# Kernel tuning notes

Hardware: AMD Instinct MI355X
Metric: run time of the kernel (lower is better)

The kernel has to match this reference:

```python
import jax, jax.numpy as jnp
import numpy as np

B, S, D, H = 2, 2048, 2048, 16
HD = D // H  # 128


def setup_inputs() -> dict:
    key = jax.random.key(0)
    ks = jax.random.split(key, 5)
    x = jax.random.normal(ks[0], (B, S, D), dtype=jnp.float32)
    scale = 1.0 / np.sqrt(D)
    wq = jax.random.normal(ks[1], (D, D), dtype=jnp.float32) * scale
    wk = jax.random.normal(ks[2], (D, D), dtype=jnp.float32) * scale
    wv = jax.random.normal(ks[3], (D, D), dtype=jnp.float32) * scale
    wo = jax.random.normal(ks[4], (D, D), dtype=jnp.float32) * scale
    # RoPE frequencies: theta = 10000, freqs_cis[t, j] = exp(i * t / theta^(2j/HD))
    inv_freq = 1.0 / (10000.0 ** (jnp.arange(0, HD, 2, dtype=jnp.float32) / HD))  # [HD/2]
    t = jnp.arange(S, dtype=jnp.float32)
    ang = jnp.outer(t, inv_freq)  # [S, HD/2]
    freqs_cos = jnp.cos(ang)
    freqs_sin = jnp.sin(ang)
    # Additive causal mask [S, S]
    neg = jnp.float32(-1e9)
    mask = jnp.triu(jnp.full((S, S), neg, dtype=jnp.float32), k=1)
    return {"x": x, "wq": wq, "wk": wk, "wv": wv, "wo": wo,
            "freqs_cos": freqs_cos, "freqs_sin": freqs_sin,
            "mask": mask, "start_pos": 0}


def _rope(t, cos, sin):
    # t: [B, S, H, HD]; cos/sin: [S, HD/2] broadcast as [1, S, 1, HD/2]
    tr = t.reshape(t.shape[:-1] + (HD // 2, 2))
    xr, xi = tr[..., 0], tr[..., 1]
    c = cos[None, :, None, :]
    s = sin[None, :, None, :]
    out_r = xr * c - xi * s
    out_i = xr * s + xi * c
    return jnp.stack([out_r, out_i], axis=-1).reshape(t.shape)


def reference(x, wq, wk, wv, wo, freqs_cos, freqs_sin, mask, start_pos):
    bsz, seqlen, _ = x.shape
    # nn.Linear: y = x @ W.T
    xq = jnp.einsum('bsd,ed->bse', x, wq).reshape(bsz, seqlen, H, HD)
    xk = jnp.einsum('bsd,ed->bse', x, wk).reshape(bsz, seqlen, H, HD)
    xv = jnp.einsum('bsd,ed->bse', x, wv).reshape(bsz, seqlen, H, HD)
    xq = _rope(xq, freqs_cos, freqs_sin)
    xk = _rope(xk, freqs_cos, freqs_sin)
    # [B, H, S, HD]
    xq = xq.transpose(0, 2, 1, 3)
    xk = xk.transpose(0, 2, 1, 3)
    xv = xv.transpose(0, 2, 1, 3)
    scores = jnp.einsum('bhqd,bhkd->bhqk', xq, xk) / jnp.sqrt(jnp.float32(HD))
    scores = scores + mask[None, None, :, :]
    probs = jax.nn.softmax(scores.astype(jnp.float32), axis=-1).astype(xq.dtype)
    out = jnp.einsum('bhqk,bhkd->bhqd', probs, xv)
    out = out.transpose(0, 2, 1, 3).reshape(bsz, seqlen, H * HD)
    return jnp.einsum('bse,de->bsd', out, wo)
```

## Files before the change

### kernel.cpp

```cpp
#include <hip/hip_runtime.h>


#define SQ 2048
#define DQ 2048
#define HQ 16
#define HDQ 128

typedef short bf16x8 __attribute__((ext_vector_type(8)));
typedef short bf16x4 __attribute__((ext_vector_type(4)));
typedef float f32x4 __attribute__((ext_vector_type(4)));

#define WAITVM4 asm volatile("s_waitcnt vmcnt(4)" ::: "memory")
#define WAITVM0 asm volatile("s_waitcnt vmcnt(0)" ::: "memory")

__device__ __forceinline__ short f2bf(float f) {
  union { float f; unsigned u; } v; v.f = f;
  unsigned r = (v.u + 0x7FFFu + ((v.u >> 16) & 1u)) >> 16;
  return (short)r;
}
__device__ __forceinline__ float bf2f(short b) {
  union { unsigned u; float f; } v; v.u = ((unsigned)(unsigned short)b) << 16;
  return v.f;
}
__device__ __forceinline__ void gload_lds16(const void* g, void* l) {
  __builtin_amdgcn_global_load_lds(
      (const __attribute__((address_space(1))) void*)g,
      (__attribute__((address_space(3))) void*)l, 16, 0, 0);
}

__global__ void cvt_kernel(const float* __restrict__ in, short* __restrict__ out, int nvec) {
  int i = blockIdx.x * blockDim.x + threadIdx.x;
  if (i >= nvec) return;
  const f32x4* p = (const f32x4*)in + (size_t)i * 2;
  f32x4 a = p[0], b = p[1];
  bf16x8 o;
  o[0] = f2bf(a[0]); o[1] = f2bf(a[1]); o[2] = f2bf(a[2]); o[3] = f2bf(a[3]);
  o[4] = f2bf(b[0]); o[5] = f2bf(b[1]); o[6] = f2bf(b[2]); o[7] = f2bf(b[3]);
  *((bf16x8*)out + i) = o;
}

__global__ void rope_kernel(short* __restrict__ t, const float* __restrict__ cosT,
                            const float* __restrict__ sinT, float scale, int nvec) {
  int i = blockIdx.x * blockDim.x + threadIdx.x;
  if (i >= nvec) return;
  size_t off = (size_t)i * 8;
  int hd0 = (int)(off & 127);
  int s = (int)((off >> 7) & 2047);
  bf16x8 v = *((const bf16x8*)(t + off));
  f32x4 c  = *(const f32x4*)(cosT + (size_t)s * 64 + (hd0 >> 1));
  f32x4 sn = *(const f32x4*)(sinT + (size_t)s * 64 + (hd0 >> 1));
  bf16x8 o;
#pragma unroll
  for (int p = 0; p < 4; ++p) {
    float xr = bf2f(v[2 * p]), xi = bf2f(v[2 * p + 1]);
    o[2 * p]     = f2bf((xr * c[p] - xi * sn[p]) * scale);
    o[2 * p + 1] = f2bf((xr * sn[p] + xi * c[p]) * scale);
  }
  *((bf16x8*)(t + off)) = o;
}

__global__ void vtrans_kernel(const short* __restrict__ vb, short* __restrict__ vtb) {
  __shared__ __align__(16) short tile[64][72];
  int bh = blockIdx.z, s0 = blockIdx.y * 64, d0 = blockIdx.x * 64;
  int tid = threadIdx.x;
#pragma unroll
  for (int it = 0; it < 2; ++it) {
    int vi = it * 256 + tid;
    int r = vi >> 3, c8 = (vi & 7) * 8;
    bf16x8 v = *(const bf16x8*)&vb[((size_t)bh * SQ + s0 + r) * HDQ + d0 + c8];
    *(bf16x8*)&tile[r][c8] = v;
  }
  __syncthreads();
#pragma unroll
  for (int it = 0; it < 2; ++it) {
    int vi = it * 256 + tid;
    int d = vi >> 3, s8 = (vi & 7) * 8;
    bf16x8 o;
#pragma unroll
    for (int j = 0; j < 8; ++j) o[j] = tile[s8 + j][d];
    *(bf16x8*)&vtb[((size_t)bh * HDQ + d0 + d) * SQ + s0 + s8] = o;
  }
}

template <int MODE>
__global__ __launch_bounds__(256, 2) void gemm_bt(const short* __restrict__ A,
                                                  const short* __restrict__ W,
                                                  short* __restrict__ oQ, short* __restrict__ oK,
                                                  short* __restrict__ oV, float* __restrict__ oF) {
  const int K = DQ;
  __shared__ __align__(16) short As[128 * 32];
  __shared__ __align__(16) short Bs[128 * 32];
  int n0 = blockIdx.x * 128, m0 = blockIdx.y * 128;
  const short* Bw = (MODE == 0) ? (W + (size_t)blockIdx.z * DQ * DQ) : W;
  int tid = threadIdx.x, w = tid >> 6, lane = tid & 63;
  int wr = w >> 1, wc = w & 1;
  int ar = lane >> 2, acol = (lane & 3) * 8;
  f32x4 acc[4][4] = {};
  int lra = wr * 64 + (lane & 15), lrb = wc * 64 + (lane & 15), kc = (lane >> 4) * 8;
  for (int k0 = 0; k0 < K; k0 += 32) {
    __syncthreads();
#pragma unroll
    for (int i = 0; i < 2; ++i) {
      int c = w * 2 + i;
      int r = c * 16 + ar;
      gload_lds16(A + (size_t)(m0 + r) * K + k0 + acol, &As[c * 512]);
      gload_lds16(Bw + (size_t)(n0 + r) * K + k0 + acol, &Bs[c * 512]);
    }
    __syncthreads();
    bf16x8 af[4], bfr[4];
#pragma unroll
    for (int f = 0; f < 4; ++f) {
      af[f] = *(const bf16x8*)&As[(lra + f * 16) * 32 + kc];
      bfr[f] = *(const bf16x8*)&Bs[(lrb + f * 16) * 32 + kc];
    }
#pragma unroll
    for (int mf = 0; mf < 4; ++mf)
#pragma unroll
      for (int nf = 0; nf < 4; ++nf)
        acc[mf][nf] = __builtin_amdgcn_mfma_f32_16x16x32_bf16(af[mf], bfr[nf], acc[mf][nf], 0, 0, 0);
  }
  short* oT = nullptr;
  if (MODE == 0) oT = (blockIdx.z == 0) ? oQ : (blockIdx.z == 1) ? oK : oV;
#pragma unroll
  for (int mf = 0; mf < 4; ++mf) {
    int mb = m0 + wr * 64 + mf * 16 + (lane >> 4) * 4;
#pragma unroll
    for (int nf = 0; nf < 4; ++nf) {
      int n = n0 + wc * 64 + nf * 16 + (lane & 15);
#pragma unroll
      for (int j = 0; j < 4; ++j) {
        int m = mb + j;
        float v = acc[mf][nf][j];
        if (MODE == 0) {
          int b = m >> 11, s = m & 2047, h = n >> 7, hd = n & 127;
          oT[(((size_t)(b * HQ + h)) * SQ + s) * HDQ + hd] = f2bf(v);
        } else {
          oF[(size_t)m * DQ + n] = v;
        }
      }
    }
  }
}

__device__ __forceinline__ void stage_kv32(const short* kbase, const short* vbase, int k0,
                                           short* KsB, short* VtB, int w, int lane) {
#pragma unroll
  for (int i = 0; i < 2; ++i) {
    int c = i * 4 + w;
    int ch = c * 64 + lane;
    int r = ch >> 4, c8 = (ch & 15) * 8;
    gload_lds16(kbase + (size_t)(k0 + r) * HDQ + (c8 ^ ((r & 7) << 3)), KsB + c * 512);
    int d = ch >> 2, k8 = (ch & 3) * 8;
    gload_lds16(vbase + (size_t)d * SQ + k0 + (k8 ^ (((d >> 1) & 3) << 3)), VtB + c * 512);
  }
}

__global__ __launch_bounds__(256, 4) void flash_kernel(const short* __restrict__ qb,
                                                       const short* __restrict__ kb,
                                                       const short* __restrict__ vtb,
                                                       short* __restrict__ ab) {
  __shared__ __align__(16) short Ks[2][32 * 128];
  __shared__ __align__(16) short Vt[2][128 * 32];
  __shared__ __align__(16) short Pl[4][16 * 32];
  int x = blockIdx.x, bh = blockIdx.y;
  int qt = (bh & 8) ? (31 - x) : x;
  int q0 = qt * 64;
  int tid = threadIdx.x, w = tid >> 6, lane = tid & 63;
  int g = lane >> 4, qcol = lane & 15;
  int qw0 = q0 + w * 16;
  const short* qbase = qb + (size_t)bh * SQ * HDQ;
  const short* kbase = kb + (size_t)bh * SQ * HDQ;
  const short* vbase = vtb + (size_t)bh * HDQ * SQ;
  int b = bh >> 4, h = bh & 15;

  bf16x8 qf[4];
#pragma unroll
  for (int cc = 0; cc < 4; ++cc)
    qf[cc] = *(const bf16x8*)&qbase[(size_t)(qw0 + qcol) * HDQ + cc * 32 + g * 8];

  f32x4 oacc[8] = {};
  float m_st = -1e30f, l_st = 0.f;
  int nt = 2 * qt + 2;
  stage_kv32(kbase, vbase, 0, Ks[0], Vt[0], w, lane);
#pragma unroll 1
  for (int t = 0; t < nt; ++t) {
    int cur = t & 1;
    int k0 = t * 32;
    __builtin_amdgcn_s_barrier();
    if (t + 1 < nt) {
      stage_kv32(kbase, vbase, (t + 1) * 32, Ks[cur ^ 1], Vt[cur ^ 1], w, lane);
      WAITVM4;
    } else {
      WAITVM0;
    }
    __builtin_amdgcn_s_barrier();
    if (k0 > qw0 + 15) continue;
    f32x4 sacc[2] = {};
    __builtin_amdgcn_s_setprio(1);
#pragma unroll
    for (int nf = 0; nf < 2; ++nf) {
      int rk = nf * 16 + qcol;
#pragma unroll
      for (int cc = 0; cc < 4; ++cc) {
        int ck = cc * 32 + g * 8;
        bf16x8 kf = *(const bf16x8*)&Ks[cur][rk * 128 + (ck ^ ((rk & 7) << 3))];
        sacc[nf] = __builtin_amdgcn_mfma_f32_16x16x32_bf16(kf, qf[cc], sacc[nf], 0, 0, 0);
      }
    }
    __builtin_amdgcn_s_setprio(0);
    int q = qw0 + qcol;
    if (k0 + 31 > qw0) {
#pragma unroll
      for (int nf = 0; nf < 2; ++nf)
#pragma unroll
        for (int j = 0; j < 4; ++j) {
          int k = k0 + nf * 16 + g * 4 + j;
          if (k > q) sacc[nf][j] = -1e9f;
        }
    }
    float mt = fmaxf(fmaxf(fmaxf(sacc[0][0], sacc[0][1]), fmaxf(sacc[0][2], sacc[0][3])),
                     fmaxf(fmaxf(sacc[1][0], sacc[1][1]), fmaxf(sacc[1][2], sacc[1][3])));
    mt = fmaxf(mt, __shfl_xor(mt, 16));
    mt = fmaxf(mt, __shfl_xor(mt, 32));
    float mn = fmaxf(m_st, mt);
    float al = exp2f(m_st - mn);
    float p0[4], p1[4];
    float ls = 0.f;
#pragma unroll
    for (int j = 0; j < 4; ++j) { p0[j] = exp2f(sacc[0][j] - mn); ls += p0[j]; }
#pragma unroll
    for (int j = 0; j < 4; ++j) { p1[j] = exp2f(sacc[1][j] - mn); ls += p1[j]; }
    l_st = l_st * al + ls;
    m_st = mn;
    int sw = (qcol & 3) * 8;
    {
      bf16x4 pk;
      pk[0] = f2bf(p0[0]); pk[1] = f2bf(p0[1]); pk[2] = f2bf(p0[2]); pk[3] = f2bf(p0[3]);
      *(bf16x4*)&Pl[w][qcol * 32 + ((g * 4) ^ sw)] = pk;
      pk[0] = f2bf(p1[0]); pk[1] = f2bf(p1[1]); pk[2] = f2bf(p1[2]); pk[3] = f2bf(p1[3]);
      *(bf16x4*)&Pl[w][qcol * 32 + ((16 + g * 4) ^ sw)] = pk;
    }
    f32x4 alv;
    alv[0] = __shfl(al, g * 4 + 0);
    alv[1] = __shfl(al, g * 4 + 1);
    alv[2] = __shfl(al, g * 4 + 2);
    alv[3] = __shfl(al, g * 4 + 3);
#pragma unroll
    for (int df = 0; df < 8; ++df) oacc[df] *= alv;
    bf16x8 pf = *(const bf16x8*)&Pl[w][qcol * 32 + ((g * 8) ^ sw)];
    __builtin_amdgcn_s_setprio(1);
#pragma unroll
    for (int df = 0; df < 8; ++df) {
      int rd = df * 16 + qcol;
      bf16x8 vf = *(const bf16x8*)&Vt[cur][rd * 32 + ((g * 8) ^ (((rd >> 1) & 3) << 3))];
      oacc[df] = __builtin_amdgcn_mfma_f32_16x16x32_bf16(pf, vf, oacc[df], 0, 0, 0);
    }
    __builtin_amdgcn_s_setprio(0);
  }
  l_st += __shfl_xor(l_st, 16);
  l_st += __shfl_xor(l_st, 32);
  float inv = 1.0f / l_st;
  f32x4 invv;
  invv[0] = __shfl(inv, g * 4 + 0);
  invv[1] = __shfl(inv, g * 4 + 1);
  invv[2] = __shfl(inv, g * 4 + 2);
  invv[3] = __shfl(inv, g * 4 + 3);
#pragma unroll
  for (int df = 0; df < 8; ++df)
#pragma unroll
    for (int j = 0; j < 4; ++j) {
      int qq = qw0 + g * 4 + j;
      int dd = df * 16 + qcol;
      ab[((size_t)b * SQ + qq) * DQ + h * HDQ + dd] = f2bf(oacc[df][j] * invv[j]);
    }
}

extern "C" void kernel_launch(void* const* d_in, const int* in_sizes, int n_in,
                              void* d_out, int out_size, void* d_ws, size_t ws_size,
                              hipStream_t stream) {
  (void)in_sizes; (void)n_in; (void)out_size; (void)ws_size;
  const float* x  = (const float*)d_in[0];
  const float* wq = (const float*)d_in[1];
  const float* wk = (const float*)d_in[2];
  const float* wv = (const float*)d_in[3];
  const float* wo = (const float*)d_in[4];
  const float* fc = (const float*)d_in[5];
  const float* fs = (const float*)d_in[6];
  float* out = (float*)d_out;

  short* xb  = (short*)d_ws;
  short* wqb = xb + (size_t)8388608;
  short* wkb = wqb + (size_t)4194304;
  short* wvb = wkb + (size_t)4194304;
  short* wob = wvb + (size_t)4194304;
  short* qb  = wob + (size_t)4194304;
  short* kb  = qb + (size_t)8388608;
  short* ab  = kb + (size_t)8388608;
  short* vb  = (short*)d_out;
  short* vtb = vb + (size_t)8388608;

  cvt_kernel<<<4096, 256, 0, stream>>>(x, xb, 1048576);
  cvt_kernel<<<2048, 256, 0, stream>>>(wq, wqb, 524288);
  cvt_kernel<<<2048, 256, 0, stream>>>(wk, wkb, 524288);
  cvt_kernel<<<2048, 256, 0, stream>>>(wv, wvb, 524288);
  cvt_kernel<<<2048, 256, 0, stream>>>(wo, wob, 524288);

  gemm_bt<0><<<dim3(16, 32, 3), 256, 0, stream>>>(xb, wqb, qb, kb, vb, nullptr);

  rope_kernel<<<4096, 256, 0, stream>>>(qb, fc, fs, 0.12751744779976827f, 1048576);
  rope_kernel<<<4096, 256, 0, stream>>>(kb, fc, fs, 1.0f, 1048576);

  vtrans_kernel<<<dim3(2, 32, 32), 256, 0, stream>>>(vb, vtb);

  flash_kernel<<<dim3(32, 32), 256, 0, stream>>>(qb, kb, vtb, ab);

  gemm_bt<1><<<dim3(16, 32, 1), 256, 0, stream>>>(ab, wob, nullptr, nullptr, nullptr, out);
}
```

Baseline: 308.8 us.

## Restructure projection GEMMs into 8-wave double-buffered 128x256 tiles with swizzled LDS

Replaces the 4-wave 128x128 GEMM, which used BK=32 and two barriers per step, with a 512-thread kernel computing 128x256 tiles at BK=64. Shared memory is double-buffered so the next K tile loads while the current one computes, synchronised with vmcnt waits. An XOR swizzle on the LDS layout avoids bank conflicts, and s_setprio is raised around the MFMA bursts. This targets global-load latency and LDS stalls in the QKV and output projections. The cost is one block per CU, fewer blocks overall, and more LDS per block.

```diff
diff --git a/kernel.cpp b/kernel.cpp
--- a/kernel.cpp
+++ b/kernel.cpp
@@ -10,6 +10,7 @@
 typedef short bf16x4 __attribute__((ext_vector_type(4)));
 typedef float f32x4 __attribute__((ext_vector_type(4)));
 
+#define WAITVM6 asm volatile("s_waitcnt vmcnt(6)" ::: "memory")
 #define WAITVM4 asm volatile("s_waitcnt vmcnt(4)" ::: "memory")
 #define WAITVM0 asm volatile("s_waitcnt vmcnt(0)" ::: "memory")
 
@@ -83,41 +84,95 @@
 }
 
 template <int MODE>
-__global__ __launch_bounds__(256, 2) void gemm_bt(const short* __restrict__ A,
-                                                  const short* __restrict__ W,
-                                                  short* __restrict__ oQ, short* __restrict__ oK,
-                                                  short* __restrict__ oV, float* __restrict__ oF) {
+__global__ __launch_bounds__(512, 1) void gemm8(const short* __restrict__ A,
+                                                const short* __restrict__ W,
+                                                short* __restrict__ oQ, short* __restrict__ oK,
+                                                short* __restrict__ oV, float* __restrict__ oF) {
+  __shared__ __align__(16) short As[2][128 * 64];
+  __shared__ __align__(16) short Bs[2][256 * 64];
   const int K = DQ;
-  __shared__ __align__(16) short As[128 * 32];
-  __shared__ __align__(16) short Bs[128 * 32];
-  int n0 = blockIdx.x * 128, m0 = blockIdx.y * 128;
+  int n0 = blockIdx.x * 256, m0 = blockIdx.y * 128;
   const short* Bw = (MODE == 0) ? (W + (size_t)blockIdx.z * DQ * DQ) : W;
-  int tid = threadIdx.x, w = tid >> 6, lane = tid & 63;
-  int wr = w >> 1, wc = w & 1;
-  int ar = lane >> 2, acol = (lane & 3) * 8;
+  int tid = threadIdx.x, wid = tid >> 6, lane = tid & 63;
+  int wr = wid >> 2, wc = wid & 3;
   f32x4 acc[4][4] = {};
-  int lra = wr * 64 + (lane & 15), lrb = wc * 64 + (lane & 15), kc = (lane >> 4) * 8;
-  for (int k0 = 0; k0 < K; k0 += 32) {
-    __syncthreads();
+
+  auto stage = [&](int kt, int buf) {
 #pragma unroll
     for (int i = 0; i < 2; ++i) {
-      int c = w * 2 + i;
-      int r = c * 16 + ar;
-      gload_lds16(A + (size_t)(m0 + r) * K + k0 + acol, &As[c * 512]);
-      gload_lds16(Bw + (size_t)(n0 + r) * K + k0 + acol, &Bs[c * 512]);
-    }
-    __syncthreads();
-    bf16x8 af[4], bfr[4];
-#pragma unroll
-    for (int f = 0; f < 4; ++f) {
-      af[f] = *(const bf16x8*)&As[(lra + f * 16) * 32 + kc];
-      bfr[f] = *(const bf16x8*)&Bs[(lrb + f * 16) * 32 + kc];
-    }
-#pragma unroll
-    for (int mf = 0; mf < 4; ++mf)
+      int g = i * 512 + tid;
+      int r = g >> 3, gg = g & 7;
+      gload_lds16(A + (size_t)(m0 + r) * K + kt * 64 + ((gg ^ (r & 7)) * 8),
+                  &As[buf][i * 4096 + wid * 512]);
+    }
+#pragma unroll
+    for (int i = 0; i < 4; ++i) {
+      int g = i * 512 + tid;
+      int r = g >> 3, gg = g & 7;
+      gload_lds16(Bw + (size_t)(n0 + r) * K + kt * 64 + ((gg ^ (r & 7)) * 8),
+                  &Bs[buf][i * 4096 + wid * 512]);
+    }
+  };
+
+  const int NT = K / 64;
+  stage(0, 0);
+#pragma unroll 1
+  for (int kt = 0; kt < NT; ++kt) {
+    int cur = kt & 1;
+    if (kt + 1 < NT) {
+      stage(kt + 1, cur ^ 1);
+      WAITVM6;
+    } else {
+      WAITVM0;
+    }
+    __builtin_amdgcn_s_barrier();
+    bf16x8 bfr[4][2], af[2][2];
+#pragma unroll
+    for (int nf = 0; nf < 4; ++nf)
+#pragma unroll
+      for (int kk = 0; kk < 2; ++kk) {
+        int br = wc * 64 + nf * 16 + (lane & 15);
+        int q = kk * 4 + (lane >> 4);
+        bfr[nf][kk] = *(const bf16x8*)&Bs[cur][br * 64 + ((q ^ (br & 7)) * 8)];
+      }
+#pragma unroll
+    for (int mf = 0; mf < 2; ++mf)
+#pragma unroll
+      for (int kk = 0; kk < 2; ++kk) {
+        int ar = wr * 64 + mf * 16 + (lane & 15);
+        int q = kk * 4 + (lane >> 4);
+        af[mf][kk] = *(const bf16x8*)&As[cur][ar * 64 + ((q ^ (ar & 7)) * 8)];
+      }
+    __builtin_amdgcn_s_setprio(1);
+#pragma unroll
+    for (int mf = 0; mf < 2; ++mf)
 #pragma unroll
       for (int nf = 0; nf < 4; ++nf)
-        acc[mf][nf] = __builtin_amdgcn_mfma_f32_16x16x32_bf16(af[mf], bfr[nf], acc[mf][nf], 0, 0, 0);
+#pragma unroll
+        for (int kk = 0; kk < 2; ++kk)
+          acc[mf][nf] = __builtin_amdgcn_mfma_f32_16x16x32_bf16(af[mf][kk], bfr[nf][kk],
+                                                                acc[mf][nf], 0, 0, 0);
+    __builtin_amdgcn_s_setprio(0);
+    __builtin_amdgcn_s_barrier();
+#pragma unroll
+    for (int mf = 0; mf < 2; ++mf)
+#pragma unroll
+      for (int kk = 0; kk < 2; ++kk) {
+        int ar = wr * 64 + (2 + mf) * 16 + (lane & 15);
+        int q = kk * 4 + (lane >> 4);
+        af[mf][kk] = *(const bf16x8*)&As[cur][ar * 64 + ((q ^ (ar & 7)) * 8)];
+      }
+    __builtin_amdgcn_s_setprio(1);
+#pragma unroll
+    for (int mf = 0; mf < 2; ++mf)
+#pragma unroll
+      for (int nf = 0; nf < 4; ++nf)
+#pragma unroll
+        for (int kk = 0; kk < 2; ++kk)
+          acc[2 + mf][nf] = __builtin_amdgcn_mfma_f32_16x16x32_bf16(af[mf][kk], bfr[nf][kk],
+                                                                    acc[2 + mf][nf], 0, 0, 0);
+    __builtin_amdgcn_s_setprio(0);
+    __builtin_amdgcn_s_barrier();
   }
   short* oT = nullptr;
   if (MODE == 0) oT = (blockIdx.z == 0) ? oQ : (blockIdx.z == 1) ? oK : oV;
@@ -305,7 +360,7 @@
   cvt_kernel<<<2048, 256, 0, stream>>>(wv, wvb, 524288);
   cvt_kernel<<<2048, 256, 0, stream>>>(wo, wob, 524288);
 
-  gemm_bt<0><<<dim3(16, 32, 3), 256, 0, stream>>>(xb, wqb, qb, kb, vb, nullptr);
+  gemm8<0><<<dim3(8, 32, 3), 512, 0, stream>>>(xb, wqb, qb, kb, vb, nullptr);
 
   rope_kernel<<<4096, 256, 0, stream>>>(qb, fc, fs, 0.12751744779976827f, 1048576);
   rope_kernel<<<4096, 256, 0, stream>>>(kb, fc, fs, 1.0f, 1048576);
@@ -314,5 +369,5 @@
 
   flash_kernel<<<dim3(32, 32), 256, 0, stream>>>(qb, kb, vtb, ab);
 
-  gemm_bt<1><<<dim3(16, 32, 1), 256, 0, stream>>>(ab, wob, nullptr, nullptr, nullptr, out);
-}
+  gemm8<1><<<dim3(8, 32, 1), 512, 0, stream>>>(ab, wob, nullptr, nullptr, nullptr, out);
+}
```

Result: slower. 346.5 us (+12.2%).

## Replace QKV projection GEMM with 256x256 triple-buffered tiled kernel

Applied to the files above, without the earlier changes.

The fused QKV projection now uses a new 512-thread kernel with 256x256 output tiles, a three-stage LDS ring of async global-to-LDS loads, XOR-swizzled LDS layout, and a grouped block-index swizzle for L2 locality. It treats the three weight matrices as one contiguous N=6144 operand and picks the Q/K/V output by column block. The aim is more data reuse per loaded tile and overlap of loads with MFMA work, replacing the 128x128 tile kernel that synced twice per k-step with no prefetch. In exchange it uses more LDS and registers, runs one workgroup per CU, and launches only 384 workgroups, which may balance poorly across CUs.

```diff
diff --git a/kernel.cpp b/kernel.cpp
--- a/kernel.cpp
+++ b/kernel.cpp
@@ -83,15 +83,126 @@
 }
 
 template <int MODE>
-__global__ __launch_bounds__(256, 2) void gemm_bt(const short* __restrict__ A,
+__global__ __launch_bounds__(512, 1) void gemm256(const short* __restrict__ A,
                                                   const short* __restrict__ W,
                                                   short* __restrict__ oQ, short* __restrict__ oK,
                                                   short* __restrict__ oV, float* __restrict__ oF) {
+  __shared__ __align__(16) short As[3][256 * 32];
+  __shared__ __align__(16) short Bs[3][256 * 32];
+  const int K = DQ;
+  const int NT = K / 32;
+  const int NBX = (MODE == 0) ? 24 : 8;
+  int nwg = gridDim.x, cpx = nwg >> 3;
+  int swz = (blockIdx.x & 7) * cpx + (blockIdx.x >> 3);
+  int bx = swz % NBX, by = swz / NBX;
+  int m0 = by * 256, n0 = bx * 256;
+  int tid = threadIdx.x, wid = tid >> 6, lane = tid & 63;
+  int wr = wid >> 2, wc = wid & 3;
+  f32x4 acc[8][4] = {};
+
+  auto stageA = [&](int kt, int buf) {
+#pragma unroll
+    for (int i = 0; i < 2; ++i) {
+      int g = i * 512 + tid;
+      int r = g >> 2, q = g & 3;
+      gload_lds16(A + (size_t)(m0 + r) * K + kt * 32 + ((q ^ (((r >> 3) & 1) << 1)) * 8),
+                  &As[buf][i * 4096 + wid * 512]);
+    }
+  };
+  auto stageB = [&](int kt, int buf) {
+#pragma unroll
+    for (int i = 0; i < 2; ++i) {
+      int g = i * 512 + tid;
+      int r = g >> 2, q = g & 3;
+      gload_lds16(W + (size_t)(n0 + r) * K + kt * 32 + ((q ^ (((r >> 3) & 1) << 1)) * 8),
+                  &Bs[buf][i * 4096 + wid * 512]);
+    }
+  };
+
+  stageA(0, 0); stageB(0, 0);
+  stageA(1, 1); stageB(1, 1);
+  WAITVM4;
+  __builtin_amdgcn_s_barrier();
+
+  int cc = (lane >> 4) * 8;
+  int cur = 0, nbuf = 2;
+#pragma unroll 1
+  for (int t = 0; t < NT; ++t) {
+    bool st = (t + 2) < NT;
+    bf16x8 bfr[4], af[4];
+#pragma unroll
+    for (int nf = 0; nf < 4; ++nf) {
+      int br = wc * 64 + nf * 16 + (lane & 15);
+      bfr[nf] = *(const bf16x8*)&Bs[cur][br * 32 + (cc ^ (((br >> 3) & 1) << 4))];
+    }
+#pragma unroll
+    for (int i = 0; i < 4; ++i) {
+      int fr = wr * 128 + i * 16 + (lane & 15);
+      af[i] = *(const bf16x8*)&As[cur][fr * 32 + (cc ^ (((fr >> 3) & 1) << 4))];
+    }
+    if (st) stageA(t + 2, nbuf);
+    __builtin_amdgcn_s_barrier();
+    __builtin_amdgcn_s_setprio(1);
+#pragma unroll
+    for (int i = 0; i < 4; ++i)
+#pragma unroll
+      for (int nf = 0; nf < 4; ++nf)
+        acc[i][nf] = __builtin_amdgcn_mfma_f32_16x16x32_bf16(af[i], bfr[nf], acc[i][nf], 0, 0, 0);
+    __builtin_amdgcn_s_setprio(0);
+    __builtin_amdgcn_s_barrier();
+#pragma unroll
+    for (int i = 0; i < 4; ++i) {
+      int fr = wr * 128 + 64 + i * 16 + (lane & 15);
+      af[i] = *(const bf16x8*)&As[cur][fr * 32 + (cc ^ (((fr >> 3) & 1) << 4))];
+    }
+    if (st) stageB(t + 2, nbuf);
+    __builtin_amdgcn_s_barrier();
+    __builtin_amdgcn_s_setprio(1);
+#pragma unroll
+    for (int i = 0; i < 4; ++i)
+#pragma unroll
+      for (int nf = 0; nf < 4; ++nf)
+        acc[4 + i][nf] = __builtin_amdgcn_mfma_f32_16x16x32_bf16(af[i], bfr[nf], acc[4 + i][nf], 0, 0, 0);
+    __builtin_amdgcn_s_setprio(0);
+    if (st) { WAITVM4; } else { WAITVM0; }
+    __builtin_amdgcn_s_barrier();
+    cur = (cur == 2) ? 0 : cur + 1;
+    nbuf = (nbuf == 2) ? 0 : nbuf + 1;
+  }
+  short* oT = nullptr;
+  int ncol0 = n0 & 2047;
+  if (MODE == 0) {
+    int zsel = n0 >> 11;
+    oT = (zsel == 0) ? oQ : (zsel == 1) ? oK : oV;
+  }
+#pragma unroll
+  for (int mf = 0; mf < 8; ++mf) {
+    int mb = m0 + wr * 128 + mf * 16 + (lane >> 4) * 4;
+#pragma unroll
+    for (int nf = 0; nf < 4; ++nf) {
+      int n = ncol0 + wc * 64 + nf * 16 + (lane & 15);
+#pragma unroll
+      for (int j = 0; j < 4; ++j) {
+        int m = mb + j;
+        float v = acc[mf][nf][j];
+        if (MODE == 0) {
+          int b = m >> 11, s = m & 2047, h = n >> 7, hd = n & 127;
+          oT[(((size_t)(b * HQ + h)) * SQ + s) * HDQ + hd] = f2bf(v);
+        } else {
+          oF[(size_t)m * DQ + (n0 + wc * 64 + nf * 16 + (lane & 15))] = v;
+        }
+      }
+    }
+  }
+}
+
+__global__ __launch_bounds__(256, 2) void gemm_bt(const short* __restrict__ A,
+                                                  const short* __restrict__ W,
+                                                  float* __restrict__ oF) {
   const int K = DQ;
   __shared__ __align__(16) short As[128 * 32];
   __shared__ __align__(16) short Bs[128 * 32];
   int n0 = blockIdx.x * 128, m0 = blockIdx.y * 128;
-  const short* Bw = (MODE == 0) ? (W + (size_t)blockIdx.z * DQ * DQ) : W;
   int tid = threadIdx.x, w = tid >> 6, lane = tid & 63;
   int wr = w >> 1, wc = w & 1;
   int ar = lane >> 2, acol = (lane & 3) * 8;
@@ -104,7 +215,7 @@
       int c = w * 2 + i;
       int r = c * 16 + ar;
       gload_lds16(A + (size_t)(m0 + r) * K + k0 + acol, &As[c * 512]);
-      gload_lds16(Bw + (size_t)(n0 + r) * K + k0 + acol, &Bs[c * 512]);
+      gload_lds16(W + (size_t)(n0 + r) * K + k0 + acol, &Bs[c * 512]);
     }
     __syncthreads();
     bf16x8 af[4], bfr[4];
@@ -119,8 +230,6 @@
       for (int nf = 0; nf < 4; ++nf)
         acc[mf][nf] = __builtin_amdgcn_mfma_f32_16x16x32_bf16(af[mf], bfr[nf], acc[mf][nf], 0, 0, 0);
   }
-  short* oT = nullptr;
-  if (MODE == 0) oT = (blockIdx.z == 0) ? oQ : (blockIdx.z == 1) ? oK : oV;
 #pragma unroll
   for (int mf = 0; mf < 4; ++mf) {
     int mb = m0 + wr * 64 + mf * 16 + (lane >> 4) * 4;
@@ -128,16 +237,8 @@
     for (int nf = 0; nf < 4; ++nf) {
       int n = n0 + wc * 64 + nf * 16 + (lane & 15);
 #pragma unroll
-      for (int j = 0; j < 4; ++j) {
-        int m = mb + j;
-        float v = acc[mf][nf][j];
-        if (MODE == 0) {
-          int b = m >> 11, s = m & 2047, h = n >> 7, hd = n & 127;
-          oT[(((size_t)(b * HQ + h)) * SQ + s) * HDQ + hd] = f2bf(v);
-        } else {
-          oF[(size_t)m * DQ + n] = v;
-        }
-      }
+      for (int j = 0; j < 4; ++j)
+        oF[(size_t)(mb + j) * DQ + n] = acc[mf][nf][j];
     }
   }
 }
@@ -175,8 +276,8 @@
 
   bf16x8 qf[4];
 #pragma unroll
-  for (int cc = 0; cc < 4; ++cc)
-    qf[cc] = *(const bf16x8*)&qbase[(size_t)(qw0 + qcol) * HDQ + cc * 32 + g * 8];
+  for (int ccq = 0; ccq < 4; ++ccq)
+    qf[ccq] = *(const bf16x8*)&qbase[(size_t)(qw0 + qcol) * HDQ + ccq * 32 + g * 8];
 
   f32x4 oacc[8] = {};
   float m_st = -1e30f, l_st = 0.f;
@@ -201,10 +302,10 @@
     for (int nf = 0; nf < 2; ++nf) {
       int rk = nf * 16 + qcol;
 #pragma unroll
-      for (int cc = 0; cc < 4; ++cc) {
-        int ck = cc * 32 + g * 8;
+      for (int ccq = 0; ccq < 4; ++ccq) {
+        int ck = ccq * 32 + g * 8;
         bf16x8 kf = *(const bf16x8*)&Ks[cur][rk * 128 + (ck ^ ((rk & 7) << 3))];
-        sacc[nf] = __builtin_amdgcn_mfma_f32_16x16x32_bf16(kf, qf[cc], sacc[nf], 0, 0, 0);
+        sacc[nf] = __builtin_amdgcn_mfma_f32_16x16x32_bf16(kf, qf[ccq], sacc[nf], 0, 0, 0);
       }
     }
     __builtin_amdgcn_s_setprio(0);
@@ -305,7 +406,7 @@
   cvt_kernel<<<2048, 256, 0, stream>>>(wv, wvb, 524288);
   cvt_kernel<<<2048, 256, 0, stream>>>(wo, wob, 524288);
 
-  gemm_bt<0><<<dim3(16, 32, 3), 256, 0, stream>>>(xb, wqb, qb, kb, vb, nullptr);
+  gemm256<0><<<dim3(384), 512, 0, stream>>>(xb, wqb, qb, kb, vb, nullptr);
 
   rope_kernel<<<4096, 256, 0, stream>>>(qb, fc, fs, 0.12751744779976827f, 1048576);
   rope_kernel<<<4096, 256, 0, stream>>>(kb, fc, fs, 1.0f, 1048576);
@@ -314,5 +415,5 @@
 
   flash_kernel<<<dim3(32, 32), 256, 0, stream>>>(qb, kb, vtb, ab);
 
-  gemm_bt<1><<<dim3(16, 32, 1), 256, 0, stream>>>(ab, wob, nullptr, nullptr, nullptr, out);
-}
+  gemm_bt<<<dim3(16, 32, 1), 256, 0, stream>>>(ab, wob, out);
+}
```

Result: no change. 313.1 us (+1.4%).

## Rewrite projection GEMMs with triple-buffered LDS pipeline, swizzle, and fused QKV grid

Applied to the files above, without the earlier changes.

Replaces the GEMM kernel with a 512-thread version that uses three LDS buffers with two tiles of prefetch in flight, waits on counted vmcnt instead of full syncthreads, and XOR-swizzles the LDS layout. The QKV projection becomes one wide GEMM with 192-wide N tiles over the concatenated weights, and a 1D grid is remapped so neighbouring blocks share tiles. The intent is to hide global-load latency, cut LDS bank conflicts and improve cache reuse in the two projection GEMMs, which are a large share of runtime. In exchange it uses more LDS and depends on the concatenated-weight layout (wq, wk, wv stored back to back) and on hand-tuned wait counts.

```diff
diff --git a/kernel.cpp b/kernel.cpp
--- a/kernel.cpp
+++ b/kernel.cpp
@@ -11,6 +11,8 @@
 typedef float f32x4 __attribute__((ext_vector_type(4)));
 
 #define WAITVM4 asm volatile("s_waitcnt vmcnt(4)" ::: "memory")
+#define WAITVM3 asm volatile("s_waitcnt vmcnt(3)" ::: "memory")
+#define WAITVM2 asm volatile("s_waitcnt vmcnt(2)" ::: "memory")
 #define WAITVM0 asm volatile("s_waitcnt vmcnt(0)" ::: "memory")
 
 __device__ __forceinline__ short f2bf(float f) {
@@ -82,60 +84,97 @@
   }
 }
 
-template <int MODE>
-__global__ __launch_bounds__(256, 2) void gemm_bt(const short* __restrict__ A,
-                                                  const short* __restrict__ W,
-                                                  short* __restrict__ oQ, short* __restrict__ oK,
-                                                  short* __restrict__ oV, float* __restrict__ oF) {
+template <int BN, int MODE>
+__global__ __launch_bounds__(512, 4) void gemmT(const short* __restrict__ A,
+                                                const short* __restrict__ W,
+                                                short* __restrict__ oQ, short* __restrict__ oK,
+                                                short* __restrict__ oV, float* __restrict__ oF) {
+  constexpr int NFR = BN / 64;
+  constexpr int NIB = BN / 16;
+  constexpr int NBX = (MODE == 0) ? (6144 / BN) : (2048 / BN);
+  __shared__ __align__(16) short As[3][128 * 32];
+  __shared__ __align__(16) short Bs[3][BN * 32];
   const int K = DQ;
-  __shared__ __align__(16) short As[128 * 32];
-  __shared__ __align__(16) short Bs[128 * 32];
-  int n0 = blockIdx.x * 128, m0 = blockIdx.y * 128;
-  const short* Bw = (MODE == 0) ? (W + (size_t)blockIdx.z * DQ * DQ) : W;
-  int tid = threadIdx.x, w = tid >> 6, lane = tid & 63;
-  int wr = w >> 1, wc = w & 1;
-  int ar = lane >> 2, acol = (lane & 3) * 8;
-  f32x4 acc[4][4] = {};
-  int lra = wr * 64 + (lane & 15), lrb = wc * 64 + (lane & 15), kc = (lane >> 4) * 8;
-  for (int k0 = 0; k0 < K; k0 += 32) {
-    __syncthreads();
-#pragma unroll
-    for (int i = 0; i < 2; ++i) {
-      int c = w * 2 + i;
-      int r = c * 16 + ar;
-      gload_lds16(A + (size_t)(m0 + r) * K + k0 + acol, &As[c * 512]);
-      gload_lds16(Bw + (size_t)(n0 + r) * K + k0 + acol, &Bs[c * 512]);
-    }
-    __syncthreads();
-    bf16x8 af[4], bfr[4];
-#pragma unroll
-    for (int f = 0; f < 4; ++f) {
-      af[f] = *(const bf16x8*)&As[(lra + f * 16) * 32 + kc];
-      bfr[f] = *(const bf16x8*)&Bs[(lrb + f * 16) * 32 + kc];
-    }
-#pragma unroll
-    for (int mf = 0; mf < 4; ++mf)
-#pragma unroll
-      for (int nf = 0; nf < 4; ++nf)
-        acc[mf][nf] = __builtin_amdgcn_mfma_f32_16x16x32_bf16(af[mf], bfr[nf], acc[mf][nf], 0, 0, 0);
-  }
-  short* oT = nullptr;
-  if (MODE == 0) oT = (blockIdx.z == 0) ? oQ : (blockIdx.z == 1) ? oK : oV;
+  const int NT = K / 32;
+  int nwg = gridDim.x, cpx = nwg >> 3;
+  int swz = (blockIdx.x & 7) * cpx + (blockIdx.x >> 3);
+  int bx = swz % NBX, by = swz / NBX;
+  int m0 = by * 128, n0 = bx * BN;
+  int tid = threadIdx.x, wid = tid >> 6, lane = tid & 63;
+  int wr = wid >> 2, wc = wid & 3;
+  f32x4 acc[4][NFR] = {};
+
+  auto stageA = [&](int kt, int buf) {
+    int g = wid * 64 + lane;
+    int r = g >> 2, q = g & 3;
+    gload_lds16(A + (size_t)(m0 + r) * K + kt * 32 + ((q ^ (((r >> 3) & 1) << 1)) * 8),
+                &As[buf][wid * 512]);
+  };
+  auto stageB = [&](int kt, int buf) {
+#pragma unroll
+    for (int i = wid; i < NIB; i += 8) {
+      int g = i * 64 + lane;
+      int r = g >> 2, q = g & 3;
+      gload_lds16(W + (size_t)(n0 + r) * K + kt * 32 + ((q ^ (((r >> 3) & 1) << 1)) * 8),
+                  &Bs[buf][i * 512]);
+    }
+  };
+
+  stageA(0, 0); stageB(0, 0);
+  stageA(1, 1); stageB(1, 1);
+  if (BN == 192 && wid < 4) { WAITVM3; } else { WAITVM2; }
+  __builtin_amdgcn_s_barrier();
+
+  int cc = (lane >> 4) * 8;
+  int cur = 0, nbuf = 2;
+#pragma unroll 1
+  for (int t = 0; t < NT; ++t) {
+    bool st = (t + 2) < NT;
+    bf16x8 bfr[NFR], af[4];
+#pragma unroll
+    for (int nf = 0; nf < NFR; ++nf) {
+      int br = wc * (BN / 4) + nf * 16 + (lane & 15);
+      bfr[nf] = *(const bf16x8*)&Bs[cur][br * 32 + (cc ^ (((br >> 3) & 1) << 4))];
+    }
+#pragma unroll
+    for (int i = 0; i < 4; ++i) {
+      int fr = wr * 64 + i * 16 + (lane & 15);
+      af[i] = *(const bf16x8*)&As[cur][fr * 32 + (cc ^ (((fr >> 3) & 1) << 4))];
+    }
+    if (st) { stageA(t + 2, nbuf); stageB(t + 2, nbuf); }
+    __builtin_amdgcn_s_setprio(1);
+#pragma unroll
+    for (int i = 0; i < 4; ++i)
+#pragma unroll
+      for (int nf = 0; nf < NFR; ++nf)
+        acc[i][nf] = __builtin_amdgcn_mfma_f32_16x16x32_bf16(af[i], bfr[nf], acc[i][nf], 0, 0, 0);
+    __builtin_amdgcn_s_setprio(0);
+    if (st) {
+      if (BN == 192 && wid < 4) { WAITVM3; } else { WAITVM2; }
+    } else {
+      WAITVM0;
+    }
+    __builtin_amdgcn_s_barrier();
+    cur = (cur == 2) ? 0 : cur + 1;
+    nbuf = (nbuf == 2) ? 0 : nbuf + 1;
+  }
 #pragma unroll
   for (int mf = 0; mf < 4; ++mf) {
     int mb = m0 + wr * 64 + mf * 16 + (lane >> 4) * 4;
 #pragma unroll
-    for (int nf = 0; nf < 4; ++nf) {
-      int n = n0 + wc * 64 + nf * 16 + (lane & 15);
+    for (int nf = 0; nf < NFR; ++nf) {
+      int n_lin = n0 + wc * (BN / 4) + nf * 16 + (lane & 15);
 #pragma unroll
       for (int j = 0; j < 4; ++j) {
         int m = mb + j;
         float v = acc[mf][nf][j];
         if (MODE == 0) {
-          int b = m >> 11, s = m & 2047, h = n >> 7, hd = n & 127;
+          int zsel = n_lin >> 11, col = n_lin & 2047;
+          short* oT = (zsel == 0) ? oQ : (zsel == 1) ? oK : oV;
+          int b = m >> 11, s = m & 2047, h = col >> 7, hd = col & 127;
           oT[(((size_t)(b * HQ + h)) * SQ + s) * HDQ + hd] = f2bf(v);
         } else {
-          oF[(size_t)m * DQ + n] = v;
+          oF[(size_t)m * DQ + n_lin] = v;
         }
       }
     }
@@ -175,8 +214,8 @@
 
   bf16x8 qf[4];
 #pragma unroll
-  for (int cc = 0; cc < 4; ++cc)
-    qf[cc] = *(const bf16x8*)&qbase[(size_t)(qw0 + qcol) * HDQ + cc * 32 + g * 8];
+  for (int ccq = 0; ccq < 4; ++ccq)
+    qf[ccq] = *(const bf16x8*)&qbase[(size_t)(qw0 + qcol) * HDQ + ccq * 32 + g * 8];
 
   f32x4 oacc[8] = {};
   float m_st = -1e30f, l_st = 0.f;
@@ -201,10 +240,10 @@
     for (int nf = 0; nf < 2; ++nf) {
       int rk = nf * 16 + qcol;
 #pragma unroll
-      for (int cc = 0; cc < 4; ++cc) {
-        int ck = cc * 32 + g * 8;
+      for (int ccq = 0; ccq < 4; ++ccq) {
+        int ck = ccq * 32 + g * 8;
         bf16x8 kf = *(const bf16x8*)&Ks[cur][rk * 128 + (ck ^ ((rk & 7) << 3))];
-        sacc[nf] = __builtin_amdgcn_mfma_f32_16x16x32_bf16(kf, qf[cc], sacc[nf], 0, 0, 0);
+        sacc[nf] = __builtin_amdgcn_mfma_f32_16x16x32_bf16(kf, qf[ccq], sacc[nf], 0, 0, 0);
       }
     }
     __builtin_amdgcn_s_setprio(0);
@@ -305,7 +344,7 @@
   cvt_kernel<<<2048, 256, 0, stream>>>(wv, wvb, 524288);
   cvt_kernel<<<2048, 256, 0, stream>>>(wo, wob, 524288);
 
-  gemm_bt<0><<<dim3(16, 32, 3), 256, 0, stream>>>(xb, wqb, qb, kb, vb, nullptr);
+  gemmT<192, 0><<<dim3(1024), 512, 0, stream>>>(xb, wqb, qb, kb, vb, nullptr);
 
   rope_kernel<<<4096, 256, 0, stream>>>(qb, fc, fs, 0.12751744779976827f, 1048576);
   rope_kernel<<<4096, 256, 0, stream>>>(kb, fc, fs, 1.0f, 1048576);
@@ -314,5 +353,5 @@
 
   flash_kernel<<<dim3(32, 32), 256, 0, stream>>>(qb, kb, vtb, ab);
 
-  gemm_bt<1><<<dim3(16, 32, 1), 256, 0, stream>>>(ab, wob, nullptr, nullptr, nullptr, out);
-}
+  gemmT<128, 1><<<dim3(512), 512, 0, stream>>>(ab, wob, nullptr, nullptr, nullptr, out);
+}
```

New measurement: 293.9 us. 4.8% less time.
